# Optimization experiments

Measured on AMD Instinct MI355X. Metric: run time of the kernel, lower is better.

The kernel has to match this reference:

```python
import jax, jax.numpy as jnp
import numpy as np

B, N, L, C, H = 4, 4096, 1024, 1024, 16
D = C // H  # head_dim = 64
SCALE = 1.0 / np.sqrt(D)


def setup_inputs() -> dict:
    key = jax.random.key(0)
    ks = jax.random.split(key, 5)
    return {
        "x": jax.random.normal(ks[0], (B, N, C), dtype=jnp.float32),
        "query": jax.random.normal(ks[1], (B, L, C), dtype=jnp.float32),
        "Wq": jax.random.normal(ks[2], (C, C), dtype=jnp.float32) * 0.02,
        "Wkv": jax.random.normal(ks[3], (2 * C, C), dtype=jnp.float32) * 0.02,
        "Wproj": jax.random.normal(ks[4], (C, C), dtype=jnp.float32) * 0.02,
        "bproj": jnp.zeros((C,), dtype=jnp.float32),
    }


def reference(x, query, Wq, Wkv, Wproj, bproj):
    # q projection: [B,L,C] -> [B,H,L,D]
    q = (query @ Wq.T).reshape(B, L, H, D).transpose(0, 2, 1, 3)
    # kv projection: [B,N,2C] -> k,v each [B,H,N,D]
    kv = (x @ Wkv.T).reshape(B, N, 2, H, D).transpose(2, 0, 3, 1, 4)
    k, v = kv[0], kv[1]
    # unfused SDPA: explicit [B,H,L,N] score matrix (faithful to source)
    attn = jnp.einsum('bhld,bhnd->bhln', q, k) * SCALE
    attn = jax.nn.softmax(attn, axis=-1)
    out = jnp.einsum('bhln,bhnd->bhld', attn, v)  # [B,H,L,D]
    out = out.transpose(0, 2, 1, 3).reshape(B, L, C)
    return out @ Wproj.T + bproj
```

## Files before the change

kernel.cpp:

```cpp
#include <hip/hip_runtime.h>
#include <hip/hip_bf16.h>

typedef __attribute__((ext_vector_type(8))) short short8;
typedef __attribute__((ext_vector_type(4))) float floatx4;

#if __has_builtin(__builtin_amdgcn_exp2f)
#define EXP2(x) __builtin_amdgcn_exp2f(x)
#else
#define EXP2(x) exp2f(x)
#endif

#define BAR() __builtin_amdgcn_s_barrier()
#define FENCE() asm volatile("" ::: "memory")
#define WAIT_LGKM0() asm volatile("s_waitcnt lgkmcnt(0)" ::: "memory")
#define WAIT_VM(n) asm volatile("s_waitcnt vmcnt(" #n ")" ::: "memory")

__device__ __forceinline__ short f2bf(float f) {
  __hip_bfloat16 h = __float2bfloat16(f);
  return *reinterpret_cast<const short*>(&h);
}

__device__ __forceinline__ short8 cvt_f32x8_bf16(const float* __restrict__ p) {
  float4 a = *reinterpret_cast<const float4*>(p);
  float4 b = *reinterpret_cast<const float4*>(p + 4);
  short8 r;
  r[0] = f2bf(a.x); r[1] = f2bf(a.y); r[2] = f2bf(a.z); r[3] = f2bf(a.w);
  r[4] = f2bf(b.x); r[5] = f2bf(b.y); r[6] = f2bf(b.z); r[7] = f2bf(b.w);
  return r;
}

typedef const __attribute__((address_space(1))) void* gptr1;
typedef __attribute__((address_space(3))) void* lptr3;
__device__ __forceinline__ void gl_lds16(const void* g, void* l) {
  __builtin_amdgcn_global_load_lds((gptr1)g, (lptr3)l, 16, 0, 0);
}

__global__ __launch_bounds__(256)
void conv_all(const float* __restrict__ x, const float* __restrict__ Wkv,
              const float* __restrict__ Wq, const float* __restrict__ Wproj,
              short* __restrict__ xb, short* __restrict__ wkvb,
              short* __restrict__ wqb, short* __restrict__ wprojb) {
  const float* src; short* dst; size_t off;
  int bi = blockIdx.x;
  int i = bi * 256 + threadIdx.x;
  if (bi < 8192)      { src = x;     dst = xb;     off = i; }
  else if (bi < 9216) { src = Wkv;   dst = wkvb;   off = i - 8192 * 256; }
  else if (bi < 9728) { src = Wq;    dst = wqb;    off = i - 9216 * 256; }
  else                { src = Wproj; dst = wprojb; off = i - 9728 * 256; }
  short8 v = cvt_f32x8_bf16(src + off * 8);
  *reinterpret_cast<short8*>(dst + off * 8) = v;
}

__global__ __launch_bounds__(512, 2)
void gemm256_kv(const short* __restrict__ A, const short* __restrict__ B,
                short* __restrict__ k_out, short* __restrict__ vt,
                int M, int N, int K)
{
  __shared__ __align__(16) short lds[2][2][2][128 * 64];

  const int tid  = threadIdx.x;
  const int lane = tid & 63;
  const int w    = tid >> 6;
  const int wm   = w >> 2;
  const int wn   = w & 3;
  const int cl   = lane & 15;
  const int hi   = lane >> 4;
  const int srl  = lane >> 3;
  const int gch8 = (((lane & 7) ^ srl) << 3);

  const int ntile = N >> 8;
  int bid = blockIdx.x;
  { int cpx = gridDim.x >> 3; bid = (bid & 7) * cpx + (bid >> 3); }
  const int tm = bid / ntile, tn = bid % ntile;
  const int m0 = tm << 8, n0 = tn << 8;
  const int NT = K >> 6;

  auto stageA = [&](int par, int slot, int ktX) {
    #pragma unroll
    for (int j = 0; j < 2; ++j) {
      const int sr = (w << 4) + (j << 3) + srl;
      const int tr = ((sr >> 6) << 7) + (slot << 6) + (sr & 63);
      gl_lds16(A + (size_t)(m0 + tr) * K + ktX + gch8,
               (void*)&lds[par][0][slot][((w << 4) + (j << 3)) * 64]);
    }
  };
  auto stageB = [&](int par, int slot, int ktX) {
    #pragma unroll
    for (int j = 0; j < 2; ++j) {
      const int sr = (w << 4) + (j << 3) + srl;
      const int tr = ((sr >> 5) << 6) + (slot << 5) + (sr & 31);
      gl_lds16(B + (size_t)(n0 + tr) * K + ktX + gch8,
               (void*)&lds[par][1][slot][((w << 4) + (j << 3)) * 64]);
    }
  };

  const floatx4 fzero = {0.f, 0.f, 0.f, 0.f};
  floatx4 acc[8][4];
  #pragma unroll
  for (int m = 0; m < 8; ++m)
    #pragma unroll
    for (int n = 0; n < 4; ++n)
      acc[m][n] = fzero;

  short8 af[4][2], b0[2][2], b1[2][2];

  auto readA = [&](int par, int slot) {
    #pragma unroll
    for (int m = 0; m < 4; ++m)
      #pragma unroll
      for (int ks = 0; ks < 2; ++ks) {
        const int sr = (wm << 6) + (m << 4) + cl;
        const int cpos = ((((ks << 2) + hi) ^ (sr & 7)) << 3);
        af[m][ks] = *reinterpret_cast<const short8*>(&lds[par][0][slot][sr * 64 + cpos]);
      }
  };
  auto readB = [&](int par, int slot, short8 (&bf)[2][2]) {
    #pragma unroll
    for (int n = 0; n < 2; ++n)
      #pragma unroll
      for (int ks = 0; ks < 2; ++ks) {
        const int sr = (wn << 5) + (n << 4) + cl;
        const int cpos = ((((ks << 2) + hi) ^ (sr & 7)) << 3);
        bf[n][ks] = *reinterpret_cast<const short8*>(&lds[par][1][slot][sr * 64 + cpos]);
      }
  };

  #define QUAD(BF, MH, NH)                                                     \
    __builtin_amdgcn_s_setprio(1);                                             \
    _Pragma("unroll")                                                          \
    for (int ks = 0; ks < 2; ++ks)                                             \
      _Pragma("unroll")                                                        \
      for (int m = 0; m < 4; ++m)                                              \
        _Pragma("unroll")                                                      \
        for (int n = 0; n < 2; ++n)                                            \
          acc[(MH)*4 + m][(NH)*2 + n] = __builtin_amdgcn_mfma_f32_16x16x32_bf16( \
              af[m][ks], BF[n][ks], acc[(MH)*4 + m][(NH)*2 + n], 0, 0, 0);     \
    __builtin_amdgcn_s_setprio(0);

  stageA(0, 0, 0); stageB(0, 0, 0); stageB(0, 1, 0); stageA(0, 1, 0);
  stageA(1, 0, 64); stageB(1, 0, 64); stageB(1, 1, 64);
  WAIT_VM(6); BAR(); FENCE();

  for (int t = 0; t < NT; ++t) {
    const int p  = t & 1;
    const int pn = p ^ 1;
    const int t1 = t + 1;
    const int t2 = t + 2;
    const int kt1 = t1 << 6;
    const int kt2 = t2 << 6;

    readA(p, 0); readB(p, 0, b0);
    if (t1 < NT) stageA(pn, 1, kt1);
    BAR(); WAIT_LGKM0();
    QUAD(b0, 0, 0);
    BAR(); FENCE();

    readB(p, 1, b1);
    if (t2 < NT) stageA(p, 0, kt2);
    BAR(); WAIT_LGKM0();
    QUAD(b1, 0, 1);
    BAR(); FENCE();

    readA(p, 1);
    if (t2 < NT) stageB(p, 0, kt2);
    BAR(); WAIT_LGKM0();
    QUAD(b0, 1, 0);
    BAR(); FENCE();

    if (t2 < NT) { stageB(p, 1, kt2); WAIT_VM(6); }
    else         { WAIT_VM(0); }
    BAR(); WAIT_LGKM0();
    QUAD(b1, 1, 1);
    BAR(); FENCE();
  }

  const int rq = hi << 2;
  #pragma unroll
  for (int Mi = 0; Mi < 8; ++Mi) {
    #pragma unroll
    for (int Nn = 0; Nn < 4; ++Nn) {
      const int grow = m0 + wm * 128 + Mi * 16 + rq;
      const int gcol = n0 + wn * 64 + Nn * 16 + cl;
      if (gcol < 1024) {
        #pragma unroll
        for (int i = 0; i < 4; ++i)
          k_out[(size_t)(grow + i) * 1024 + gcol] = f2bf(acc[Mi][Nn][i]);
      } else {
        const int d  = gcol - 1024;
        const int bb = grow >> 12;
        const int nn = grow & 4095;
        size_t base = ((size_t)(bb * 16 + (d >> 6)) * 64 + (d & 63)) * 4096 + nn;
        short4 pk;
        pk.x = f2bf(acc[Mi][Nn][0]); pk.y = f2bf(acc[Mi][Nn][1]);
        pk.z = f2bf(acc[Mi][Nn][2]); pk.w = f2bf(acc[Mi][Nn][3]);
        *reinterpret_cast<short4*>(&vt[base]) = pk;
      }
    }
  }
}

template<int MODE, bool AFP32>
__global__ __launch_bounds__(256, 4)
void gemm64(const void* __restrict__ Ap, const short* __restrict__ B,
            void* __restrict__ O0, const float* __restrict__ bias,
            int M, int N, int K, float oscale)
{
  __shared__ __align__(16) short As[64 * 64];
  __shared__ __align__(16) short Bs[64 * 64];

  const int tid  = threadIdx.x;
  const int lane = tid & 63;
  const int w    = tid >> 6;
  const int ntile = N >> 6;
  int bid = blockIdx.x;
  { int cpx = gridDim.x >> 3; bid = (bid & 7) * cpx + (bid >> 3); }
  const int tm = bid / ntile;
  const int tn = bid % ntile;
  const int m0 = tm << 6, n0 = tn << 6;
  const int wr = (w >> 1) << 5;
  const int wc = (w & 1) << 5;
  const int cl = lane & 15;
  const int hi = lane >> 4;
  const int srow = lane >> 3;
  const int scol = (lane & 7) << 3;

  const floatx4 fzero = {0.f, 0.f, 0.f, 0.f};
  floatx4 acc[2][2];
  #pragma unroll
  for (int m = 0; m < 2; ++m)
    #pragma unroll
    for (int n = 0; n < 2; ++n)
      acc[m][n] = fzero;

  for (int kt = 0; kt < K; kt += 64) {
    if (AFP32) {
      const float* A = (const float*)Ap;
      #pragma unroll
      for (int sgm = 0; sgm < 2; ++sgm) {
        const int seg = tid + sgm * 256;
        const int row = seg >> 3;
        const int c8  = (seg & 7) << 3;
        short8 v = cvt_f32x8_bf16(A + (size_t)(m0 + row) * K + kt + c8);
        *reinterpret_cast<short8*>(&As[row * 64 + c8]) = v;
      }
    } else {
      const short* A = (const short*)Ap;
      #pragma unroll
      for (int i = 0; i < 2; ++i) {
        const int chunk = (w << 1) + i;
        const int row   = (chunk << 3) + srow;
        gl_lds16(A + (size_t)(m0 + row) * K + kt + scol, &As[chunk * 512]);
      }
    }
    #pragma unroll
    for (int i = 0; i < 2; ++i) {
      const int chunk = (w << 1) + i;
      const int row   = (chunk << 3) + srow;
      gl_lds16(B + (size_t)(n0 + row) * K + kt + scol, &Bs[chunk * 512]);
    }
    __syncthreads();

    #pragma unroll
    for (int ks = 0; ks < 2; ++ks) {
      short8 af[2], bfr[2];
      #pragma unroll
      for (int m = 0; m < 2; ++m)
        af[m] = *reinterpret_cast<const short8*>(
            &As[(wr + m * 16 + cl) * 64 + ks * 32 + (hi << 3)]);
      #pragma unroll
      for (int n = 0; n < 2; ++n)
        bfr[n] = *reinterpret_cast<const short8*>(
            &Bs[(wc + n * 16 + cl) * 64 + ks * 32 + (hi << 3)]);
      #pragma unroll
      for (int m = 0; m < 2; ++m)
        #pragma unroll
        for (int n = 0; n < 2; ++n)
          acc[m][n] = __builtin_amdgcn_mfma_f32_16x16x32_bf16(af[m], bfr[n], acc[m][n], 0, 0, 0);
    }
    __syncthreads();
  }

  const int rq = hi << 2;
  #pragma unroll
  for (int m = 0; m < 2; ++m) {
    #pragma unroll
    for (int n = 0; n < 2; ++n) {
      const int grow = m0 + wr + m * 16 + rq;
      const int gcol = n0 + wc + n * 16 + cl;
      if (MODE == 0) {
        short* o = (short*)O0;
        #pragma unroll
        for (int i = 0; i < 4; ++i)
          o[(size_t)(grow + i) * N + gcol] = f2bf(acc[m][n][i] * oscale);
      } else {
        float* o = (float*)O0;
        const float bv = bias[gcol];
        #pragma unroll
        for (int i = 0; i < 4; ++i)
          o[(size_t)(grow + i) * N + gcol] = acc[m][n][i] + bv;
      }
    }
  }
}

__global__ __launch_bounds__(256, 3)
void attn_fwd(const short* __restrict__ q_ws, const short* __restrict__ k_ws,
              const short* __restrict__ vt_ws, short* __restrict__ ao_ws)
{
  __shared__ __align__(16) short Ks[2][64 * 64];
  __shared__ __align__(16) short Vts[2][64 * 64];
  __shared__ __align__(16) short Pl[4][32 * 64];

  const int tid  = threadIdx.x;
  const int lane = tid & 63;
  const int w    = tid >> 6;
  const int i    = blockIdx.x;
  const int bh   = (i & 7) * 8 + (i >> 6);
  const int qt   = (i >> 3) & 7;
  const int b  = bh >> 4;
  const int h  = bh & 15;
  const int q0 = qt * 128 + w * 32;
  const int cl = lane & 15;
  const int hi = lane >> 4;
  const int rq = hi << 2;
  const int key7 = cl & 7;

  short8 qf[2][2];
  #pragma unroll
  for (int tt = 0; tt < 2; ++tt)
    #pragma unroll
    for (int ks = 0; ks < 2; ++ks) {
      size_t idx = (size_t)(b * 1024 + q0 + tt * 16 + cl) * 1024
                 + h * 64 + ks * 32 + (hi << 3);
      qf[tt][ks] = *reinterpret_cast<const short8*>(&q_ws[idx]);
    }

  int koff[2];
  #pragma unroll
  for (int ks = 0; ks < 2; ++ks)
    koff[ks] = cl * 64 + ((((ks << 2) + hi) ^ key7) << 3);
  const int pwc   = hi >> 1;
  const int pwoff = (hi & 1) << 2;
  int pwch[4];
  #pragma unroll
  for (int n = 0; n < 4; ++n)
    pwch[n] = ((((n << 1) + pwc) ^ key7) << 3) + pwoff + cl * 64;

  const floatx4 fzero = {0.f, 0.f, 0.f, 0.f};
  floatx4 o[2][4];
  floatx4 ol[2];
  floatx4 s[4][2];
  short8 vones;
  #pragma unroll
  for (int j = 0; j < 8; ++j) vones[j] = (short)0x3F80;
  #pragma unroll
  for (int tt = 0; tt < 2; ++tt) {
    ol[tt] = fzero;
    #pragma unroll
    for (int nd = 0; nd < 4; ++nd) o[tt][nd] = fzero;
  }

  const int c0    = w << 1;
  const int srow8 = lane >> 3;
  const int gch8  = (((lane & 7) ^ srow8) << 3);
  const short* kbase = k_ws + (size_t)(b * 4096 + (c0 << 3) + srow8) * 1024 + h * 64 + gch8;
  const short* vbase = vt_ws + ((size_t)bh * 64 + (c0 << 3) + srow8) * 4096 + gch8;

  auto stage = [&](int buf, int kv0) {
    gl_lds16(kbase + (size_t)kv0 * 1024,          (void*)&Ks[buf][c0 * 512]);
    gl_lds16(kbase + (size_t)kv0 * 1024 + 8192,   (void*)&Ks[buf][(c0 + 1) * 512]);
    gl_lds16(vbase + kv0,                          (void*)&Vts[buf][c0 * 512]);
    gl_lds16(vbase + kv0 + 8 * 4096,               (void*)&Vts[buf][(c0 + 1) * 512]);
  };

  auto qk = [&](const short* kb) {
    short8 kf[2][4];
    #pragma unroll
    for (int ks = 0; ks < 2; ++ks)
      #pragma unroll
      for (int n = 0; n < 4; ++n)
        kf[ks][n] = *reinterpret_cast<const short8*>(kb + koff[ks] + n * 1024);
    #pragma unroll
    for (int n = 0; n < 4; ++n)
      #pragma unroll
      for (int tt = 0; tt < 2; ++tt)
        s[n][tt] = __builtin_amdgcn_mfma_f32_16x16x32_bf16(
            kf[1][n], qf[tt][1],
            __builtin_amdgcn_mfma_f32_16x16x32_bf16(kf[0][n], qf[tt][0], fzero, 0, 0, 0),
            0, 0, 0);
  };
  auto pv = [&](const short* plb, const short* vb) {
    #pragma unroll
    for (int ks = 0; ks < 2; ++ks) {
      short8 pa[2], vf[4];
      #pragma unroll
      for (int tt = 0; tt < 2; ++tt)
        pa[tt] = *reinterpret_cast<const short8*>(plb + koff[ks] + tt * 1024);
      #pragma unroll
      for (int nd = 0; nd < 4; ++nd)
        vf[nd] = *reinterpret_cast<const short8*>(vb + koff[ks] + nd * 1024);
      #pragma unroll
      for (int tt = 0; tt < 2; ++tt) {
        ol[tt] = __builtin_amdgcn_mfma_f32_16x16x32_bf16(pa[tt], vones, ol[tt], 0, 0, 0);
        #pragma unroll
        for (int nd = 0; nd < 4; ++nd)
          o[tt][nd] = __builtin_amdgcn_mfma_f32_16x16x32_bf16(pa[tt], vf[nd], o[tt][nd], 0, 0, 0);
      }
    }
  };
  auto smax = [&](short* plw) {
    #pragma unroll
    for (int tt = 0; tt < 2; ++tt)
      #pragma unroll
      for (int n = 0; n < 4; ++n) {
        short4 pk;
        #pragma unroll
        for (int ii = 0; ii < 4; ++ii)
          pk[ii] = f2bf(EXP2(s[n][tt][ii]));
        *reinterpret_cast<short4*>(plw + tt * 1024 + pwch[n]) = pk;
      }
  };

  stage(0, 0);
  WAIT_VM(0); BAR(); FENCE();
  qk(&Ks[0][0]);
  stage(1, 64);
  smax(&Pl[w][0]);

  for (int t = 0; t < 63; ++t) {
    const int cur = t & 1;
    WAIT_VM(0); BAR(); FENCE();
    __builtin_amdgcn_s_setprio(1);
    qk(&Ks[cur ^ 1][0]);
    pv(&Pl[w][0], &Vts[cur][0]);
    __builtin_amdgcn_s_setprio(0);
    FENCE(); BAR();
    stage(cur, ((t + 2) & 63) << 6);
    WAIT_LGKM0();
    smax(&Pl[w][0]);
  }
  __builtin_amdgcn_s_setprio(1);
  pv(&Pl[w][0], &Vts[1][0]);
  __builtin_amdgcn_s_setprio(0);
  WAIT_VM(0);

  #pragma unroll
  for (int m = 0; m < 2; ++m) {
    float inv[4];
    #pragma unroll
    for (int ii = 0; ii < 4; ++ii)
      inv[ii] = 1.f / ol[m][ii];
    #pragma unroll
    for (int nd = 0; nd < 4; ++nd)
      #pragma unroll
      for (int ii = 0; ii < 4; ++ii) {
        size_t idx = (size_t)(b * 1024 + q0 + m * 16 + rq + ii) * 1024
                   + h * 64 + nd * 16 + cl;
        ao_ws[idx] = f2bf(o[m][nd][ii] * inv[ii]);
      }
  }
}

extern "C" void kernel_launch(void* const* d_in, const int* in_sizes, int n_in,
                              void* d_out, int out_size, void* d_ws, size_t ws_size,
                              hipStream_t stream)
{
  const float* x     = (const float*)d_in[0];
  const float* query = (const float*)d_in[1];
  const float* Wq    = (const float*)d_in[2];
  const float* Wkv   = (const float*)d_in[3];
  const float* Wproj = (const float*)d_in[4];
  const float* bproj = (const float*)d_in[5];
  float* out = (float*)d_out;

  const float QSCALE = 0.18033688011112042f;

  char* ws = (char*)d_ws;
  short* k_ws   = (short*)(ws);
  short* vt_ws  = (short*)(ws + (32ull << 20));
  short* xb     = (short*)(ws + (64ull << 20));
  short* q_ws   = (short*)(ws + (72ull << 20));
  short* ao_ws  = (short*)(ws + (80ull << 20));
  short* wkvb   = (short*)(ws + (96ull << 20));
  short* wqb    = (short*)(ws + (100ull << 20));
  short* wprojb = (short*)(ws + (102ull << 20));

  conv_all<<<dim3(10240), 256, 0, stream>>>(x, Wkv, Wq, Wproj,
                                            xb, wkvb, wqb, wprojb);
  gemm256_kv<<<dim3(512), 512, 0, stream>>>(xb, wkvb, k_ws, vt_ws,
                                            16384, 2048, 1024);
  gemm64<0, true><<<dim3(1024), 256, 0, stream>>>(query, wqb, q_ws, nullptr,
                                                  4096, 1024, 1024, QSCALE);
  attn_fwd<<<dim3(512), 256, 0, stream>>>(q_ws, k_ws, vt_ws, ao_ws);
  gemm64<2, false><<<dim3(1024), 256, 0, stream>>>(ao_ws, wprojb, out, bproj,
                                                   4096, 1024, 1024, 1.0f);
}
```

Baseline: 214.6 us.

## Fuse x fp32-to-bf16 conversion into KV GEMM A-tile loading

Drops the separate pass that converted x (64 MB fp32) to a bf16 workspace. The KV GEMM now loads fp32 A tiles into registers, converts them, and writes them to LDS inside the existing software pipeline, and B staging is made unconditional using wrapped indices. This removes a full read/write round trip of x through memory. In exchange the GEMM reads twice as many A bytes per tile, uses more registers for the in-flight A loads, and replaces async global-to-LDS copies with register-staged writes, which may reduce overlap.

```diff
diff --git a/kernel.cpp b/kernel.cpp
--- a/kernel.cpp
+++ b/kernel.cpp
@@ -36,23 +36,20 @@
 }
 
 __global__ __launch_bounds__(256)
-void conv_all(const float* __restrict__ x, const float* __restrict__ Wkv,
-              const float* __restrict__ Wq, const float* __restrict__ Wproj,
-              short* __restrict__ xb, short* __restrict__ wkvb,
-              short* __restrict__ wqb, short* __restrict__ wprojb) {
-  const float* src; short* dst; size_t off;
-  int bi = blockIdx.x;
-  int i = bi * 256 + threadIdx.x;
-  if (bi < 8192)      { src = x;     dst = xb;     off = i; }
-  else if (bi < 9216) { src = Wkv;   dst = wkvb;   off = i - 8192 * 256; }
-  else if (bi < 9728) { src = Wq;    dst = wqb;    off = i - 9216 * 256; }
-  else                { src = Wproj; dst = wprojb; off = i - 9728 * 256; }
-  short8 v = cvt_f32x8_bf16(src + off * 8);
-  *reinterpret_cast<short8*>(dst + off * 8) = v;
+void conv_weights(const float* __restrict__ Wkv, const float* __restrict__ Wq,
+                  const float* __restrict__ Wproj, short* __restrict__ wkvb,
+                  short* __restrict__ wqb, short* __restrict__ wprojb) {
+  const float* src; short* dst; int off;
+  int i = blockIdx.x * 256 + threadIdx.x;
+  if (blockIdx.x < 1024)      { src = Wkv;   dst = wkvb;   off = i; }
+  else if (blockIdx.x < 1536) { src = Wq;    dst = wqb;    off = i - 1024 * 256; }
+  else                        { src = Wproj; dst = wprojb; off = i - 1536 * 256; }
+  short8 v = cvt_f32x8_bf16(src + (size_t)off * 8);
+  *reinterpret_cast<short8*>(dst + (size_t)off * 8) = v;
 }
 
 __global__ __launch_bounds__(512, 2)
-void gemm256_kv(const short* __restrict__ A, const short* __restrict__ B,
+void gemm256_kv(const float* __restrict__ A, const short* __restrict__ B,
                 short* __restrict__ k_out, short* __restrict__ vt,
                 int M, int N, int K)
 {
@@ -75,13 +72,27 @@
   const int m0 = tm << 8, n0 = tn << 8;
   const int NT = K >> 6;
 
-  auto stageA = [&](int par, int slot, int ktX) {
+  struct Aregs { float4 v[4]; };
+  auto loadA = [&](Aregs& r, int slot, int ktX) {
     #pragma unroll
     for (int j = 0; j < 2; ++j) {
       const int sr = (w << 4) + (j << 3) + srl;
       const int tr = ((sr >> 6) << 7) + (slot << 6) + (sr & 63);
-      gl_lds16(A + (size_t)(m0 + tr) * K + ktX + gch8,
-               (void*)&lds[par][0][slot][((w << 4) + (j << 3)) * 64]);
+      const float* p = A + (size_t)(m0 + tr) * K + ktX + gch8;
+      r.v[j * 2]     = *reinterpret_cast<const float4*>(p);
+      r.v[j * 2 + 1] = *reinterpret_cast<const float4*>(p + 4);
+    }
+  };
+  auto writeA = [&](const Aregs& r, int par, int slot) {
+    #pragma unroll
+    for (int j = 0; j < 2; ++j) {
+      const float4& a  = r.v[j * 2];
+      const float4& b2 = r.v[j * 2 + 1];
+      short8 o;
+      o[0] = f2bf(a.x);  o[1] = f2bf(a.y);  o[2] = f2bf(a.z);  o[3] = f2bf(a.w);
+      o[4] = f2bf(b2.x); o[5] = f2bf(b2.y); o[6] = f2bf(b2.z); o[7] = f2bf(b2.w);
+      *reinterpret_cast<short8*>(
+          &lds[par][0][slot][((w << 4) + (j << 3)) * 64 + lane * 8]) = o;
     }
   };
   auto stageB = [&](int par, int slot, int ktX) {
@@ -137,42 +148,48 @@
               af[m][ks], BF[n][ks], acc[(MH)*4 + m][(NH)*2 + n], 0, 0, 0);     \
     __builtin_amdgcn_s_setprio(0);
 
-  stageA(0, 0, 0); stageB(0, 0, 0); stageB(0, 1, 0); stageA(0, 1, 0);
-  stageA(1, 0, 64); stageB(1, 0, 64); stageB(1, 1, 64);
-  WAIT_VM(6); BAR(); FENCE();
-
+  {
+    Aregs pa00, pa10, pa01;
+    loadA(pa00, 0, 0); loadA(pa10, 1, 0); loadA(pa01, 0, 64);
+    stageB(0, 0, 0); stageB(0, 1, 0); stageB(1, 0, 64); stageB(1, 1, 64);
+    writeA(pa00, 0, 0); writeA(pa10, 0, 1); writeA(pa01, 1, 0);
+    WAIT_VM(0); BAR(); FENCE();
+  }
+
+  Aregs ra1, ra0;
   for (int t = 0; t < NT; ++t) {
     const int p  = t & 1;
     const int pn = p ^ 1;
     const int t1 = t + 1;
     const int t2 = t + 2;
-    const int kt1 = t1 << 6;
-    const int kt2 = t2 << 6;
+    int t2w = t2; if (t2w >= NT) t2w -= NT;
 
     readA(p, 0); readB(p, 0, b0);
-    if (t1 < NT) stageA(pn, 1, kt1);
+    if (t1 < NT) loadA(ra1, 1, t1 << 6);
     BAR(); WAIT_LGKM0();
     QUAD(b0, 0, 0);
     BAR(); FENCE();
 
     readB(p, 1, b1);
-    if (t2 < NT) stageA(p, 0, kt2);
+    if (t2 < NT) loadA(ra0, 0, t2 << 6);
     BAR(); WAIT_LGKM0();
     QUAD(b1, 0, 1);
     BAR(); FENCE();
 
     readA(p, 1);
-    if (t2 < NT) stageB(p, 0, kt2);
+    if (t1 < NT) writeA(ra1, pn, 1);
+    stageB(p, 0, t2w << 6);
     BAR(); WAIT_LGKM0();
     QUAD(b0, 1, 0);
     BAR(); FENCE();
 
-    if (t2 < NT) { stageB(p, 1, kt2); WAIT_VM(6); }
-    else         { WAIT_VM(0); }
+    if (t2 < NT) writeA(ra0, p, 0);
+    stageB(p, 1, t2w << 6);
     BAR(); WAIT_LGKM0();
     QUAD(b1, 1, 1);
     BAR(); FENCE();
   }
+  WAIT_VM(0);
 
   const int rq = hi << 2;
   #pragma unroll
@@ -234,22 +251,22 @@
 
   for (int kt = 0; kt < K; kt += 64) {
     if (AFP32) {
-      const float* A = (const float*)Ap;
+      const float* Af = (const float*)Ap;
       #pragma unroll
       for (int sgm = 0; sgm < 2; ++sgm) {
         const int seg = tid + sgm * 256;
         const int row = seg >> 3;
         const int c8  = (seg & 7) << 3;
-        short8 v = cvt_f32x8_bf16(A + (size_t)(m0 + row) * K + kt + c8);
+        short8 v = cvt_f32x8_bf16(Af + (size_t)(m0 + row) * K + kt + c8);
         *reinterpret_cast<short8*>(&As[row * 64 + c8]) = v;
       }
     } else {
-      const short* A = (const short*)Ap;
+      const short* Ab = (const short*)Ap;
       #pragma unroll
       for (int i = 0; i < 2; ++i) {
         const int chunk = (w << 1) + i;
         const int row   = (chunk << 3) + srow;
-        gl_lds16(A + (size_t)(m0 + row) * K + kt + scol, &As[chunk * 512]);
+        gl_lds16(Ab + (size_t)(m0 + row) * K + kt + scol, &As[chunk * 512]);
       }
     }
     #pragma unroll
@@ -478,16 +495,14 @@
   char* ws = (char*)d_ws;
   short* k_ws   = (short*)(ws);
   short* vt_ws  = (short*)(ws + (32ull << 20));
-  short* xb     = (short*)(ws + (64ull << 20));
-  short* q_ws   = (short*)(ws + (72ull << 20));
-  short* ao_ws  = (short*)(ws + (80ull << 20));
+  short* q_ws   = (short*)(ws + (64ull << 20));
+  short* ao_ws  = (short*)(ws + (72ull << 20));
   short* wkvb   = (short*)(ws + (96ull << 20));
   short* wqb    = (short*)(ws + (100ull << 20));
   short* wprojb = (short*)(ws + (102ull << 20));
 
-  conv_all<<<dim3(10240), 256, 0, stream>>>(x, Wkv, Wq, Wproj,
-                                            xb, wkvb, wqb, wprojb);
-  gemm256_kv<<<dim3(512), 512, 0, stream>>>(xb, wkvb, k_ws, vt_ws,
+  conv_weights<<<dim3(2048), 256, 0, stream>>>(Wkv, Wq, Wproj, wkvb, wqb, wprojb);
+  gemm256_kv<<<dim3(512), 512, 0, stream>>>(x, wkvb, k_ws, vt_ws,
                                             16384, 2048, 1024);
   gemm64<0, true><<<dim3(1024), 256, 0, stream>>>(query, wqb, q_ws, nullptr,
                                                   4096, 1024, 1024, QSCALE);
```

New measurement: 281.6 us. +31.3%, slower.
